# Kernel tuning notes

Hardware: AMD Instinct MI355X
Metric: run time of the kernel (lower is better)

## Reference

```python
import jax, jax.numpy as jnp
import numpy as np

B, N, K = 4, 2048, 32
U, TU = 512, 128
RADII = (0.1, 0.3, 0.5)
FILTERS = [512, 256, 170]  # U // (i+1) for depth=3
BN_RS = 1.0 / np.sqrt(1.0 + 1e-3)  # inference BN with mean=0, var=1, keras eps=1e-3


def setup_inputs() -> dict:
    key = jax.random.key(0)
    ks = jax.random.split(key, 16)
    rn = lambda k, shape, s: jax.random.normal(k, shape, jnp.float32) * s
    d = {
        "pts": jax.random.normal(ks[0], (B, N, 3), jnp.float32),
        # T-Net params
        "t_cw": rn(ks[1], (3, TU), 0.3), "t_cb": jnp.zeros((TU,), jnp.float32),
        "t_g1": jnp.ones((TU,), jnp.float32), "t_b1": jnp.zeros((TU,), jnp.float32),
        "t_d1w": rn(ks[2], (TU, TU), 0.1), "t_d1b": jnp.zeros((TU,), jnp.float32),
        "t_g2": jnp.ones((TU,), jnp.float32), "t_b2": jnp.zeros((TU,), jnp.float32),
        "t_d2w": rn(ks[3], (TU, 9), 0.3), "t_d2b": jnp.zeros((9,), jnp.float32),
        # PCE conv1 + residual conv
        "c1_w": rn(ks[4], (9, U), 0.2), "c1_b": jnp.zeros((U,), jnp.float32),
        "c1_g": jnp.ones((U,), jnp.float32), "c1_beta": jnp.zeros((U,), jnp.float32),
        "res_w": rn(ks[5], (U, U), 0.05), "res_b": jnp.zeros((U,), jnp.float32),
    }
    fin = U
    for i, f in enumerate(FILTERS):
        d[f"blk{i}_w"] = rn(ks[6 + i], (fin, f), 0.05)
        d[f"blk{i}_b"] = jnp.zeros((f,), jnp.float32)
        d[f"blk{i}_g"] = jnp.ones((f,), jnp.float32)
        d[f"blk{i}_beta"] = jnp.zeros((f,), jnp.float32)
        fin = f
    return d


def _bn(x, g, b):
    # inference BN with moving_mean=0, moving_var=1: (x-0)/sqrt(1+eps)*g + b
    return x * (BN_RS * g) + b


def reference(pts, t_cw, t_cb, t_g1, t_b1, t_d1w, t_d1b, t_g2, t_b2, t_d2w, t_d2b,
              c1_w, c1_b, c1_g, c1_beta, res_w, res_b,
              blk0_w, blk0_b, blk0_g, blk0_beta,
              blk1_w, blk1_b, blk1_g, blk1_beta,
              blk2_w, blk2_b, blk2_g, blk2_beta):
    silu = jax.nn.silu  # keras 'swish'
    # ---- OrthogonalTNet (dropout = identity at inference) ----
    x = silu(_bn(jnp.einsum('bnd,de->bne', pts, t_cw) + t_cb, t_g1, t_b1))  # [B,N,TU]
    x = x.max(axis=1)                                                        # GlobalMaxPool1D
    x = silu(_bn(x @ t_d1w + t_d1b, t_g2, t_b2))
    T = (x @ t_d2w + t_d2b).reshape(-1, 3, 3)
    pc = jnp.einsum('bnd,bde->bne', pts, T)                                  # [B,N,3]
    # ---- pairwise distances [B,N,N] ----
    sq = jnp.sum(pc * pc, axis=-1)
    d2 = sq[:, :, None] + sq[:, None, :] - 2.0 * jnp.einsum('bnd,bmd->bnm', pc, pc)
    dist = jnp.sqrt(jnp.maximum(d2, 0.0))
    # ---- multi-scale grouping: radius mask -> top_k -> gather ----
    groups = []
    for r in RADII:
        mask = (dist <= r).astype(jnp.float32)
        idx = jax.lax.top_k(mask, K)[1]                                      # [B,N,K]
        groups.append(jax.vmap(lambda p, i: p[i])(pc, idx))                  # [B,N,K,3]
    f = jnp.concatenate(groups, axis=-1)                                     # [B,N,K,9]
    # ---- 1x1 conv stack (Dense over channel dim), dropout = identity ----
    f = silu(_bn(f @ c1_w + c1_b, c1_g, c1_beta))                            # [B,N,K,U]
    f = f + (f @ res_w + res_b)                                              # residual
    for w, b, g, beta in ((blk0_w, blk0_b, blk0_g, blk0_beta),
                          (blk1_w, blk1_b, blk1_g, blk1_beta),
                          (blk2_w, blk2_b, blk2_g, blk2_beta)):
        f = silu(_bn(f @ w + b, g, beta))
    Bv, Nv, Kv, Cv = f.shape
    f = f.reshape(Bv, Nv, Kv * Cv)                                           # [B,N,K*170]
    return f.max(axis=1)                                                     # GlobalMaxPool1D -> [B,5440]
```

## Files before the change

kernel.cpp:

```cpp
#include <hip/hip_runtime.h>
#include <math.h>

#define BN_RS 0.9995003746877732f

typedef unsigned short u16;
typedef _Float16 f16;
typedef __attribute__((ext_vector_type(8))) _Float16 h8v;
typedef __attribute__((ext_vector_type(4))) _Float16 h4v;
typedef __attribute__((ext_vector_type(2))) __fp16 fp16x2;
typedef __attribute__((ext_vector_type(4))) float f32x4;
typedef __attribute__((ext_vector_type(16))) float f32x16;

__device__ __forceinline__ unsigned f2mono(float f){
  unsigned u = __float_as_uint(f);
  return (u & 0x80000000u) ? ~u : (u | 0x80000000u);
}
__device__ __forceinline__ float mono2f(unsigned m){
  unsigned u = (m & 0x80000000u) ? (m & 0x7FFFFFFFu) : ~m;
  return __uint_as_float(u);
}
__device__ __forceinline__ float silu_fast(float x){
  float e = __expf(-x);
  return x * __builtin_amdgcn_rcpf(1.f + e);
}
__device__ __forceinline__ float silu_f64(float x){
  double e = exp(-(double)x);
  return (float)((double)x / (1.0 + e));
}
__device__ __forceinline__ h4v pkrtz4(float a, float b, float c, float d){
  fp16x2 lo = __builtin_amdgcn_cvt_pkrtz(a, b);
  fp16x2 hi = __builtin_amdgcn_cvt_pkrtz(c, d);
  unsigned lu = __builtin_bit_cast(unsigned, lo);
  unsigned hu = __builtin_bit_cast(unsigned, hi);
  unsigned long long packed = ((unsigned long long)hu << 32) | lu;
  return __builtin_bit_cast(h4v, packed);
}

constexpr size_t OFF_T9   = 0;
constexpr size_t OFF_XM   = 1024;
constexpr size_t OFF_PC4  = 4096;
constexpr size_t OFF_OUT  = 139264;
constexpr size_t OFF_C1T  = 227328;
constexpr size_t OFF_B0C  = 262144;
constexpr size_t OFF_B1T  = 1310720;
constexpr size_t OFF_B2T  = 1572864;
constexpr size_t OFF_BS1  = 1662976;
constexpr size_t OFF_BS0  = 1667072;
constexpr size_t OFF_BSB1 = 1669120;
constexpr size_t OFF_BSB2 = 1670144;
constexpr size_t OFF_F9   = 1703936;

__global__ void tnet1_kernel(const float* __restrict__ pts, const float* __restrict__ t_cw,
                             const float* __restrict__ t_cb, const float* __restrict__ t_g1,
                             const float* __restrict__ t_b1, unsigned* __restrict__ xm_mono){
  int u = threadIdx.x;
  int b = blockIdx.x;
  int slice = blockIdx.y * blockDim.y + threadIdx.y;
  float w0 = t_cw[u], w1 = t_cw[128+u], w2 = t_cw[256+u];
  float cb = t_cb[u];
  float sc = __fmul_rn(BN_RS, t_g1[u]);
  float b1 = t_b1[u];
  float mx = -INFINITY;
  const float* P = pts + ((size_t)b*2048 + (size_t)slice*128)*3;
  for (int n = 0; n < 128; ++n){
    float y = __fadd_rn(__fadd_rn(__fmul_rn(P[n*3+0], w0), __fmul_rn(P[n*3+1], w1)),
                        __fmul_rn(P[n*3+2], w2));
    y = __fadd_rn(y, cb);
    y = __fadd_rn(__fmul_rn(y, sc), b1);
    mx = fmaxf(mx, silu_f64(y));
  }
  atomicMax(&xm_mono[b*128+u], f2mono(mx));
}

__global__ void tnet2_kernel(const unsigned* __restrict__ xm_mono,
                             const float* __restrict__ d1w, const float* __restrict__ d1b,
                             const float* __restrict__ g2, const float* __restrict__ b2,
                             const float* __restrict__ d2w, const float* __restrict__ d2b,
                             float* __restrict__ T9){
  __shared__ float xs[128], x2s[128];
  int u = threadIdx.x, b = blockIdx.x;
  xs[u] = mono2f(xm_mono[b*128+u]);
  __syncthreads();
  double acc = (double)d1b[u];
  for (int v = 0; v < 128; ++v) acc += (double)xs[v] * (double)d1w[v*128+u];
  double sc = (double)__fmul_rn(BN_RS, g2[u]);
  acc = acc*sc + (double)b2[u];
  double e = exp(-acc);
  x2s[u] = (float)(acc / (1.0 + e));
  __syncthreads();
  if (u < 9){
    double t = (double)d2b[u];
    for (int v = 0; v < 128; ++v) t += (double)x2s[v] * (double)d2w[v*9+u];
    T9[b*9+u] = (float)t;
  }
}

__global__ void pc_kernel(const float* __restrict__ pts, const float* __restrict__ T9,
                          float4* __restrict__ pc4){
  int i = blockIdx.x*blockDim.x + threadIdx.x;
  int b = i >> 11;
  const float* p = pts + (size_t)i*3;
  float x = p[0], y = p[1], z = p[2];
  const float* T = T9 + b*9;
  float px = __fadd_rn(__fadd_rn(__fmul_rn(x, T[0]), __fmul_rn(y, T[3])), __fmul_rn(z, T[6]));
  float py = __fadd_rn(__fadd_rn(__fmul_rn(x, T[1]), __fmul_rn(y, T[4])), __fmul_rn(z, T[7]));
  float pz = __fadd_rn(__fadd_rn(__fmul_rn(x, T[2]), __fmul_rn(y, T[5])), __fmul_rn(z, T[8]));
  float sq = __fadd_rn(__fadd_rn(__fmul_rn(px, px), __fmul_rn(py, py)), __fmul_rn(pz, pz));
  pc4[i] = make_float4(px, py, pz, sq);
}

__global__ __launch_bounds__(256) void group_kernel(const float4* __restrict__ pc4,
                                                    f16* __restrict__ f9){
  __shared__ int ones[4][3][32];
  __shared__ int zer [4][3][32];
  const float RAD[3] = {0.1f, 0.3f, 0.5f};
  int tid = threadIdx.x, wave = tid >> 6, lane = tid & 63;
  int bid = blockIdx.x;
  int b = bid >> 9, n0 = (bid & 511) * 4;
  const float4* src = pc4 + (size_t)b*2048;

  int n = n0 + wave;
  float4 pi = src[n];
  float xi = pi.x, yi = pi.y, zi = pi.z, sqi = pi.w;
  int c1[3] = {0,0,0}, c0[3] = {0,0,0};
  unsigned long long lt = (1ULL << lane) - 1ULL;

  for (int ch = 0; ch < 32; ++ch){
    int j = ch*64 + lane;
    float4 pj = src[j];
    float dot = __fadd_rn(__fadd_rn(__fmul_rn(xi, pj.x), __fmul_rn(yi, pj.y)),
                          __fmul_rn(zi, pj.z));
    float d2 = __fsub_rn(__fadd_rn(sqi, pj.w), __fmul_rn(2.f, dot));
    float dist = sqrtf(fmaxf(d2, 0.f));
    #pragma unroll
    for (int ri = 0; ri < 3; ++ri){
      bool in = (dist <= RAD[ri]);
      unsigned long long m = __ballot(in);
      int pc_lt = (int)__popcll(m & lt);
      if (c1[ri] < 32){
        int pos = c1[ri] + pc_lt;
        if (in && pos < 32) ones[wave][ri][pos] = j;
      }
      if (c0[ri] < 32){
        int pos = c0[ri] + (int)(lane - pc_lt);
        if (!in && pos < 32) zer[wave][ri][pos] = j;
      }
      int t1 = (int)__popcll(m);
      c1[ri] += t1;
      c0[ri] += 64 - t1;
    }
    if (c1[0] >= 32 && c1[1] >= 32 && c1[2] >= 32 &&
        c0[0] >= 32 && c0[1] >= 32 && c0[2] >= 32) break;
  }

  if (lane < 32){
    h8v va, vb;
    #pragma unroll
    for (int t = 0; t < 8; ++t){ va[t] = (f16)0.f; vb[t] = (f16)0.f; }
    #pragma unroll
    for (int ri = 0; ri < 3; ++ri){
      int cc = c1[ri] < 32 ? c1[ri] : 32;
      int sel = (lane < cc) ? ones[wave][ri][lane] : zer[wave][ri][lane - cc];
      float4 p = src[sel];
      if (ri == 0){ va[0]=(f16)p.x; va[1]=(f16)p.y; va[2]=(f16)p.z; }
      if (ri == 1){ va[3]=(f16)p.x; va[4]=(f16)p.y; va[5]=(f16)p.z; }
      if (ri == 2){ va[6]=(f16)p.x; va[7]=(f16)p.y; vb[0]=(f16)p.z; }
    }
    f16* dst = f9 + (((size_t)(b*2048 + n) * 32 + lane) << 4);
    *(h8v*)dst = va;
    *(h8v*)(dst + 8) = vb;
  }
}

__device__ __forceinline__ void pack_frag32(const float* __restrict__ src, f16* __restrict__ dst,
                                            int CO, int CI, int COr, int CIr,
                                            const float* __restrict__ g,
                                            int i0, int stride){
  int NT16 = CI >> 4;
  int total = (CO >> 5) * NT16 * 512;
  for (int x = i0; x < total; x += stride){
    int j = x & 7, lane = (x >> 3) & 63;
    int t = (x >> 9) % NT16, sct = x / (NT16 << 9);
    int co = sct*32 + (lane & 31);
    int ci = t*16 + ((lane >> 5) << 3) + j;
    float v = 0.f;
    if (co < COr && ci < CIr){
      v = src[ci*COr + co];
      if (g) v *= BN_RS * g[co];
    }
    dst[x] = (f16)v;
  }
}
__device__ __forceinline__ void pack_frag16(const float* __restrict__ src, f16* __restrict__ dst,
                                            int CO, int CI, int COr, int CIr,
                                            const float* __restrict__ g,
                                            int i0, int stride){
  int NT = CI >> 5;
  int total = (CO >> 4) * NT * 512;
  for (int x = i0; x < total; x += stride){
    int j = x & 7, lane = (x >> 3) & 63;
    int t = (x >> 9) % NT, sct = x / (NT << 9);
    int co = sct*16 + (lane & 15);
    int ci = t*32 + (lane >> 4)*8 + j;
    float v = 0.f;
    if (co < COr && ci < CIr){
      v = src[ci*COr + co];
      if (g) v *= BN_RS * g[co];
    }
    dst[x] = (f16)v;
  }
}

__global__ void prep_kernel(const float* __restrict__ c1w,
                            const float* __restrict__ b0w, const float* __restrict__ b1w,
                            const float* __restrict__ b2w,
                            const float* __restrict__ c1_b, const float* __restrict__ c1_g, const float* __restrict__ c1_be,
                            const float* __restrict__ res_b,
                            const float* __restrict__ b0_b, const float* __restrict__ b0_g, const float* __restrict__ b0_be,
                            const float* __restrict__ b1_b, const float* __restrict__ b1_g, const float* __restrict__ b1_be,
                            const float* __restrict__ b2_b, const float* __restrict__ b2_g, const float* __restrict__ b2_be,
                            f16* __restrict__ c1F, f16* __restrict__ b1F, f16* __restrict__ b2F,
                            float* __restrict__ bs1, float* __restrict__ bs0,
                            float* __restrict__ bsb1, float* __restrict__ bsb2){
  int i0 = blockIdx.x*blockDim.x + threadIdx.x;
  int stride = gridDim.x*blockDim.x;
  pack_frag32(c1w,  c1F,  512,  32, 512,   9, c1_g, i0, stride);
  pack_frag32(b1w,  b1F,  256, 512, 256, 512, b1_g, i0, stride);
  pack_frag16(b2w,  b2F,  176, 256, 170, 256, b2_g, i0, stride);
  for (int x = i0; x < 512; x += stride){
    bs1[x] = c1_b[x]*(BN_RS*c1_g[x]) + c1_be[x];
    float s = b0_b[x];
    for (int m = 0; m < 512; ++m) s = fmaf(res_b[m], b0w[m*512 + x], s);
    bs0[x] = s*(BN_RS*b0_g[x]) + b0_be[x];
  }
  for (int x = i0; x < 256; x += stride) bsb1[x] = b1_b[x]*(BN_RS*b1_g[x]) + b1_be[x];
  for (int x = i0; x < 176; x += stride)
    bsb2[x] = (x < 170) ? b2_b[x]*(BN_RS*b2_g[x]) + b2_be[x] : 0.f;
}

__global__ __launch_bounds__(256) void composeb0_kernel(const float* __restrict__ resw,
                                                        const float* __restrict__ b0w,
                                                        const float* __restrict__ b0_g,
                                                        f16* __restrict__ b0C){
  __shared__ float Rt[64][129];
  __shared__ float Wt[128][17];
  const int tid = threadIdx.x;
  const int co0 = (blockIdx.x & 31) * 16;
  const int ci0 = (blockIdx.x >> 5) * 64;
  const int r  = tid >> 2;
  const int cq = tid & 3;
  float acc[4] = {0.f, 0.f, 0.f, 0.f};

  for (int mc = 0; mc < 512; mc += 128){
    {
      int row = tid >> 2, mb = (tid & 3) * 32;
      const float* src = resw + (size_t)(ci0 + row)*512 + mc + mb;
      #pragma unroll
      for (int i = 0; i < 8; ++i){
        float4 v = *(const float4*)(src + i*4);
        Rt[row][mb + i*4 + 0] = v.x; Rt[row][mb + i*4 + 1] = v.y;
        Rt[row][mb + i*4 + 2] = v.z; Rt[row][mb + i*4 + 3] = v.w;
      }
    }
    {
      int m = tid >> 1, c8 = (tid & 1) * 8;
      const float* src = b0w + (size_t)(mc + m)*512 + co0 + c8;
      float4 v0 = *(const float4*)(src);
      float4 v1 = *(const float4*)(src + 4);
      Wt[m][c8+0] = v0.x; Wt[m][c8+1] = v0.y; Wt[m][c8+2] = v0.z; Wt[m][c8+3] = v0.w;
      Wt[m][c8+4] = v1.x; Wt[m][c8+5] = v1.y; Wt[m][c8+6] = v1.z; Wt[m][c8+7] = v1.w;
    }
    __syncthreads();
    #pragma unroll 8
    for (int m = 0; m < 128; ++m){
      float rv = Rt[r][m];
      #pragma unroll
      for (int i = 0; i < 4; ++i)
        acc[i] = fmaf(rv, Wt[m][cq*4 + i], acc[i]);
    }
    __syncthreads();
  }
  int ci = ci0 + r;
  #pragma unroll
  for (int i = 0; i < 4; ++i){
    int co = co0 + cq*4 + i;
    float s = acc[i] + b0w[(size_t)ci*512 + co];
    s *= BN_RS * b0_g[co];
    int sct = co >> 5, t = ci >> 4;
    int lane = (co & 31) | (((ci >> 3) & 1) << 5);
    int j = ci & 7;
    b0C[((size_t)(sct*32 + t)*64 + lane)*8 + j] = (f16)s;
  }
}

__device__ __forceinline__ int swzb(int row, int c){
  return (row*1024 + c*2) ^ ((row & 7) << 4);
}

template<int NT16, int NCT>
__device__ __forceinline__ void mm32(const char* actc, const f16* __restrict__ WF,
                                     int sct0, int lane, f32x16 (&acc)[NCT]){
  const int ln = lane & 31, hi = lane >> 5;
  const int xr = (ln & 7) << 4;
  #pragma unroll
  for (int t = 0; t < NT16; ++t){
    int koff = (t*32 + (hi << 4)) ^ xr;
    h8v a = *(const h8v*)(actc + ln*1024 + koff);
    #pragma unroll
    for (int ct = 0; ct < NCT; ++ct){
      h8v w = *(const h8v*)&WF[((size_t)((sct0 + ct)*NT16 + t)*64 + lane)*8];
      acc[ct] = __builtin_amdgcn_mfma_f32_32x32x16_f16(w, a, acc[ct], 0, 0, 0);
    }
  }
}

template<int NCT>
__device__ __forceinline__ void epi32(char* outc, int co0, const float* __restrict__ bias,
                                      int lane, f32x16 (&acc)[NCT]){
  const int ln = lane & 31, hi = lane >> 5;
  #pragma unroll
  for (int ct = 0; ct < NCT; ++ct){
    #pragma unroll
    for (int q = 0; q < 4; ++q){
      int ch = co0 + ct*32 + q*8 + hi*4;
      float4 b4 = *(const float4*)(bias + ch);
      *(h4v*)(outc + swzb(ln, ch)) = pkrtz4(
          silu_fast(acc[ct][q*4+0] + b4.x),
          silu_fast(acc[ct][q*4+1] + b4.y),
          silu_fast(acc[ct][q*4+2] + b4.z),
          silu_fast(acc[ct][q*4+3] + b4.w));
    }
  }
}

__global__ __launch_bounds__(512, 4) void mlp_kernel(
    const f16* __restrict__ f9,
    const f16* __restrict__ c1F, const f16* __restrict__ b0C,
    const f16* __restrict__ b1F, const f16* __restrict__ b2F,
    const float* __restrict__ bs1, const float* __restrict__ bs0,
    const float* __restrict__ bsb1, const float* __restrict__ bsb2,
    unsigned* __restrict__ outmax){
  __shared__ __align__(16) f16 bufA[32*512];
  __shared__ __align__(16) f16 bufB[32*512];
  char* A = (char*)bufA;
  char* B = (char*)bufB;
  const int tid  = threadIdx.x;
  const int wave = tid >> 6, lane = tid & 63;
  const int ln = lane & 31, hi = lane >> 5;
  const int lrow = lane & 15, lkg = lane >> 4;
  const int bid = blockIdx.x;
  const int b = bid >> 11, k = (bid >> 6) & 31, n0 = (bid & 63) << 5;

  if (tid < 128){
    int row = tid >> 2, part = tid & 3;
    h8v v;
    if (part < 2){
      const f16* src = f9 + (((size_t)(b*2048 + n0 + row) * 32 + k) << 4) + part*8;
      v = *(const h8v*)src;
    } else {
      #pragma unroll
      for (int t = 0; t < 8; ++t) v[t] = (f16)0.f;
    }
    *(h8v*)&bufA[row*32 + part*8] = v;
  }
  __syncthreads();

  const f32x16 zf16 = {0.f,0.f,0.f,0.f,0.f,0.f,0.f,0.f,0.f,0.f,0.f,0.f,0.f,0.f,0.f,0.f};
  f32x16 acc[2];

  acc[0] = zf16; acc[1] = zf16;
  #pragma unroll
  for (int t = 0; t < 2; ++t){
    h8v a = *(const h8v*)(A + ln*64 + t*32 + hi*16);
    #pragma unroll
    for (int ct = 0; ct < 2; ++ct){
      h8v w = *(const h8v*)&c1F[((size_t)((wave*2 + ct)*2 + t)*64 + lane)*8];
      acc[ct] = __builtin_amdgcn_mfma_f32_32x32x16_f16(w, a, acc[ct], 0, 0, 0);
    }
  }
  epi32<2>(B, wave*64, bs1, lane, acc);
  __syncthreads();

  acc[0] = zf16; acc[1] = zf16;
  mm32<32, 2>(B, b0C, wave*2, lane, acc);
  epi32<2>(A, wave*64, bs0, lane, acc);
  __syncthreads();

  f32x16 acc1[1];
  acc1[0] = zf16;
  mm32<32, 1>(A, b1F, wave, lane, acc1);
  epi32<1>(B, wave*32, bsb1, lane, acc1);
  __syncthreads();

  const f32x4 zf = {0.f, 0.f, 0.f, 0.f};
  f32x4 acc3[2][2];
  #pragma unroll
  for (int mt = 0; mt < 2; ++mt){ acc3[mt][0] = zf; acc3[mt][1] = zf; }
  {
    const int xr = (lrow & 7) << 4;
    const bool has2 = wave < 3;
    #pragma unroll
    for (int t = 0; t < 8; ++t){
      h8v a[2];
      int koff = ((t*4 + lkg) << 4) ^ xr;
      #pragma unroll
      for (int mt = 0; mt < 2; ++mt)
        a[mt] = *(const h8v*)(B + (mt*16 + lrow)*1024 + koff);
      {
        h8v w = *(const h8v*)&b2F[((size_t)(wave*8 + t)*64 + lane)*8];
        #pragma unroll
        for (int mt = 0; mt < 2; ++mt)
          acc3[mt][0] = __builtin_amdgcn_mfma_f32_16x16x32_f16(a[mt], w, acc3[mt][0], 0, 0, 0);
      }
      if (has2){
        h8v w = *(const h8v*)&b2F[((size_t)((wave + 8)*8 + t)*64 + lane)*8];
        #pragma unroll
        for (int mt = 0; mt < 2; ++mt)
          acc3[mt][1] = __builtin_amdgcn_mfma_f32_16x16x32_f16(a[mt], w, acc3[mt][1], 0, 0, 0);
      }
    }
    #pragma unroll
    for (int t = 0; t < 2; ++t){
      if (t == 1 && !has2) break;
      int c = ((t == 0) ? wave : wave + 8)*16 + lrow;
      if (c < 170){
        float bb = bsb2[c];
        float mx = -INFINITY;
        #pragma unroll
        for (int mt = 0; mt < 2; ++mt)
          #pragma unroll
          for (int rg = 0; rg < 4; ++rg)
            mx = fmaxf(mx, silu_fast(acc3[mt][t][rg] + bb));
        mx = fmaxf(mx, __shfl_xor(mx, 16));
        mx = fmaxf(mx, __shfl_xor(mx, 32));
        if (lkg == 0)
          atomicMax(&outmax[b*5440 + k*170 + c], f2mono(mx));
      }
    }
  }
}

__global__ void finalize_kernel(const unsigned* __restrict__ m, float* __restrict__ out, int n){
  int i = blockIdx.x*blockDim.x + threadIdx.x;
  if (i < n) out[i] = mono2f(m[i]);
}

extern "C" void kernel_launch(void* const* d_in, const int* in_sizes, int n_in,
                              void* d_out, int out_size, void* d_ws, size_t ws_size,
                              hipStream_t stream){
  const float* pts    = (const float*)d_in[0];
  const float* t_cw   = (const float*)d_in[1];
  const float* t_cb   = (const float*)d_in[2];
  const float* t_g1   = (const float*)d_in[3];
  const float* t_b1   = (const float*)d_in[4];
  const float* t_d1w  = (const float*)d_in[5];
  const float* t_d1b  = (const float*)d_in[6];
  const float* t_g2   = (const float*)d_in[7];
  const float* t_b2   = (const float*)d_in[8];
  const float* t_d2w  = (const float*)d_in[9];
  const float* t_d2b  = (const float*)d_in[10];
  const float* c1_w   = (const float*)d_in[11];
  const float* c1_b   = (const float*)d_in[12];
  const float* c1_g   = (const float*)d_in[13];
  const float* c1_be  = (const float*)d_in[14];
  const float* res_w  = (const float*)d_in[15];
  const float* res_b  = (const float*)d_in[16];
  const float* b0_w   = (const float*)d_in[17];
  const float* b0_b   = (const float*)d_in[18];
  const float* b0_g   = (const float*)d_in[19];
  const float* b0_be  = (const float*)d_in[20];
  const float* b1_w   = (const float*)d_in[21];
  const float* b1_b   = (const float*)d_in[22];
  const float* b1_g   = (const float*)d_in[23];
  const float* b1_be  = (const float*)d_in[24];
  const float* b2_w   = (const float*)d_in[25];
  const float* b2_b   = (const float*)d_in[26];
  const float* b2_g   = (const float*)d_in[27];
  const float* b2_be  = (const float*)d_in[28];

  char* ws = (char*)d_ws;
  float*    T9   = (float*)(ws + OFF_T9);
  unsigned* XM   = (unsigned*)(ws + OFF_XM);
  float4*   PC4  = (float4*)(ws + OFF_PC4);
  unsigned* OUTM = (unsigned*)(ws + OFF_OUT);
  f16* C1F  = (f16*)(ws + OFF_C1T);
  f16* B0C  = (f16*)(ws + OFF_B0C);
  f16* B1F  = (f16*)(ws + OFF_B1T);
  f16* B2F  = (f16*)(ws + OFF_B2T);
  float* BS1  = (float*)(ws + OFF_BS1);
  float* BS0  = (float*)(ws + OFF_BS0);
  float* BSB1 = (float*)(ws + OFF_BSB1);
  float* BSB2 = (float*)(ws + OFF_BSB2);
  f16* F9   = (f16*)(ws + OFF_F9);

  hipMemsetAsync(ws + OFF_XM, 0, 4*128*4, stream);
  hipMemsetAsync(ws + OFF_OUT, 0, 21760*4, stream);

  prep_kernel<<<512, 256, 0, stream>>>(c1_w, b0_w, b1_w, b2_w,
                                       c1_b, c1_g, c1_be, res_b,
                                       b0_b, b0_g, b0_be,
                                       b1_b, b1_g, b1_be,
                                       b2_b, b2_g, b2_be,
                                       C1F, B1F, B2F,
                                       BS1, BS0, BSB1, BSB2);
  composeb0_kernel<<<256, 256, 0, stream>>>(res_w, b0_w, b0_g, B0C);
  tnet1_kernel<<<dim3(4,4), dim3(128,4), 0, stream>>>(pts, t_cw, t_cb, t_g1, t_b1, XM);
  tnet2_kernel<<<4, 128, 0, stream>>>(XM, t_d1w, t_d1b, t_g2, t_b2, t_d2w, t_d2b, T9);
  pc_kernel<<<32, 256, 0, stream>>>(pts, T9, PC4);
  group_kernel<<<2048, 256, 0, stream>>>(PC4, F9);
  mlp_kernel<<<8192, 512, 0, stream>>>(F9, C1F, B0C, B1F, B2F,
                                       BS1, BS0, BSB1, BSB2, OUTM);
  finalize_kernel<<<(out_size + 255)/256, 256, 0, stream>>>(OUTM, (float*)d_out, out_size);
}
```

Baseline: 466.4 us.

## Process 64 points per MLP block to reuse each weight fragment twice

Doubles the row tile of the fused MLP kernel from 32 to 64 points, so each weight fragment loaded from global memory feeds two MFMAs instead of one. The grid is halved, the shared buffers double to 64 KB each, and launch bounds drop to 2 blocks per CU. This targets weight-load bandwidth and latency in the GEMM chain, at the cost of more registers, more LDS per block and lower occupancy.

```diff
diff --git a/kernel.cpp b/kernel.cpp
--- a/kernel.cpp
+++ b/kernel.cpp
@@ -298,25 +298,27 @@
 }
 
 template<int NT16, int NCT>
-__device__ __forceinline__ void mm32(const char* actc, const f16* __restrict__ WF,
-                                     int sct0, int lane, f32x16 (&acc)[NCT]){
+__device__ __forceinline__ void mm32x2(const char* actc, const f16* __restrict__ WF,
+                                       int sct0, int lane, f32x16 (&acc)[2][NCT]){
   const int ln = lane & 31, hi = lane >> 5;
   const int xr = (ln & 7) << 4;
   #pragma unroll
   for (int t = 0; t < NT16; ++t){
     int koff = (t*32 + (hi << 4)) ^ xr;
-    h8v a = *(const h8v*)(actc + ln*1024 + koff);
+    h8v a0 = *(const h8v*)(actc + ln*1024 + koff);
+    h8v a1 = *(const h8v*)(actc + (32 + ln)*1024 + koff);
     #pragma unroll
     for (int ct = 0; ct < NCT; ++ct){
       h8v w = *(const h8v*)&WF[((size_t)((sct0 + ct)*NT16 + t)*64 + lane)*8];
-      acc[ct] = __builtin_amdgcn_mfma_f32_32x32x16_f16(w, a, acc[ct], 0, 0, 0);
+      acc[0][ct] = __builtin_amdgcn_mfma_f32_32x32x16_f16(w, a0, acc[0][ct], 0, 0, 0);
+      acc[1][ct] = __builtin_amdgcn_mfma_f32_32x32x16_f16(w, a1, acc[1][ct], 0, 0, 0);
     }
   }
 }
 
 template<int NCT>
-__device__ __forceinline__ void epi32(char* outc, int co0, const float* __restrict__ bias,
-                                      int lane, f32x16 (&acc)[NCT]){
+__device__ __forceinline__ void epi32x2(char* outc, int co0, const float* __restrict__ bias,
+                                        int lane, f32x16 (&acc)[2][NCT]){
   const int ln = lane & 31, hi = lane >> 5;
   #pragma unroll
   for (int ct = 0; ct < NCT; ++ct){
@@ -324,24 +326,28 @@
     for (int q = 0; q < 4; ++q){
       int ch = co0 + ct*32 + q*8 + hi*4;
       float4 b4 = *(const float4*)(bias + ch);
-      *(h4v*)(outc + swzb(ln, ch)) = pkrtz4(
-          silu_fast(acc[ct][q*4+0] + b4.x),
-          silu_fast(acc[ct][q*4+1] + b4.y),
-          silu_fast(acc[ct][q*4+2] + b4.z),
-          silu_fast(acc[ct][q*4+3] + b4.w));
-    }
-  }
-}
-
-__global__ __launch_bounds__(512, 4) void mlp_kernel(
+      #pragma unroll
+      for (int mt = 0; mt < 2; ++mt){
+        int row = mt*32 + ln;
+        *(h4v*)(outc + swzb(row, ch)) = pkrtz4(
+            silu_fast(acc[mt][ct][q*4+0] + b4.x),
+            silu_fast(acc[mt][ct][q*4+1] + b4.y),
+            silu_fast(acc[mt][ct][q*4+2] + b4.z),
+            silu_fast(acc[mt][ct][q*4+3] + b4.w));
+      }
+    }
+  }
+}
+
+__global__ __launch_bounds__(512, 2) void mlp_kernel(
     const f16* __restrict__ f9,
     const f16* __restrict__ c1F, const f16* __restrict__ b0C,
     const f16* __restrict__ b1F, const f16* __restrict__ b2F,
     const float* __restrict__ bs1, const float* __restrict__ bs0,
     const float* __restrict__ bsb1, const float* __restrict__ bsb2,
     unsigned* __restrict__ outmax){
-  __shared__ __align__(16) f16 bufA[32*512];
-  __shared__ __align__(16) f16 bufB[32*512];
+  __shared__ __align__(16) f16 bufA[64*512];
+  __shared__ __align__(16) f16 bufB[64*512];
   char* A = (char*)bufA;
   char* B = (char*)bufB;
   const int tid  = threadIdx.x;
@@ -349,9 +355,9 @@
   const int ln = lane & 31, hi = lane >> 5;
   const int lrow = lane & 15, lkg = lane >> 4;
   const int bid = blockIdx.x;
-  const int b = bid >> 11, k = (bid >> 6) & 31, n0 = (bid & 63) << 5;
-
-  if (tid < 128){
+  const int b = bid >> 10, k = (bid >> 5) & 31, n0 = (bid & 31) << 6;
+
+  if (tid < 256){
     int row = tid >> 2, part = tid & 3;
     h8v v;
     if (part < 2){
@@ -366,56 +372,58 @@
   __syncthreads();
 
   const f32x16 zf16 = {0.f,0.f,0.f,0.f,0.f,0.f,0.f,0.f,0.f,0.f,0.f,0.f,0.f,0.f,0.f,0.f};
-  f32x16 acc[2];
-
-  acc[0] = zf16; acc[1] = zf16;
+  f32x16 acc[2][2];
+
+  acc[0][0] = zf16; acc[0][1] = zf16; acc[1][0] = zf16; acc[1][1] = zf16;
   #pragma unroll
   for (int t = 0; t < 2; ++t){
-    h8v a = *(const h8v*)(A + ln*64 + t*32 + hi*16);
+    h8v a0 = *(const h8v*)(A + ln*64 + t*32 + hi*16);
+    h8v a1 = *(const h8v*)(A + (32 + ln)*64 + t*32 + hi*16);
     #pragma unroll
     for (int ct = 0; ct < 2; ++ct){
       h8v w = *(const h8v*)&c1F[((size_t)((wave*2 + ct)*2 + t)*64 + lane)*8];
-      acc[ct] = __builtin_amdgcn_mfma_f32_32x32x16_f16(w, a, acc[ct], 0, 0, 0);
-    }
-  }
-  epi32<2>(B, wave*64, bs1, lane, acc);
+      acc[0][ct] = __builtin_amdgcn_mfma_f32_32x32x16_f16(w, a0, acc[0][ct], 0, 0, 0);
+      acc[1][ct] = __builtin_amdgcn_mfma_f32_32x32x16_f16(w, a1, acc[1][ct], 0, 0, 0);
+    }
+  }
+  epi32x2<2>(B, wave*64, bs1, lane, acc);
   __syncthreads();
 
-  acc[0] = zf16; acc[1] = zf16;
-  mm32<32, 2>(B, b0C, wave*2, lane, acc);
-  epi32<2>(A, wave*64, bs0, lane, acc);
+  acc[0][0] = zf16; acc[0][1] = zf16; acc[1][0] = zf16; acc[1][1] = zf16;
+  mm32x2<32, 2>(B, b0C, wave*2, lane, acc);
+  epi32x2<2>(A, wave*64, bs0, lane, acc);
   __syncthreads();
 
-  f32x16 acc1[1];
-  acc1[0] = zf16;
-  mm32<32, 1>(A, b1F, wave, lane, acc1);
-  epi32<1>(B, wave*32, bsb1, lane, acc1);
+  f32x16 acc1[2][1];
+  acc1[0][0] = zf16; acc1[1][0] = zf16;
+  mm32x2<32, 1>(A, b1F, wave, lane, acc1);
+  epi32x2<1>(B, wave*32, bsb1, lane, acc1);
   __syncthreads();
 
   const f32x4 zf = {0.f, 0.f, 0.f, 0.f};
-  f32x4 acc3[2][2];
+  f32x4 acc3[4][2];
   #pragma unroll
-  for (int mt = 0; mt < 2; ++mt){ acc3[mt][0] = zf; acc3[mt][1] = zf; }
+  for (int mt = 0; mt < 4; ++mt){ acc3[mt][0] = zf; acc3[mt][1] = zf; }
   {
     const int xr = (lrow & 7) << 4;
     const bool has2 = wave < 3;
     #pragma unroll
     for (int t = 0; t < 8; ++t){
-      h8v a[2];
+      h8v a[4];
       int koff = ((t*4 + lkg) << 4) ^ xr;
       #pragma unroll
-      for (int mt = 0; mt < 2; ++mt)
+      for (int mt = 0; mt < 4; ++mt)
         a[mt] = *(const h8v*)(B + (mt*16 + lrow)*1024 + koff);
       {
         h8v w = *(const h8v*)&b2F[((size_t)(wave*8 + t)*64 + lane)*8];
         #pragma unroll
-        for (int mt = 0; mt < 2; ++mt)
+        for (int mt = 0; mt < 4; ++mt)
           acc3[mt][0] = __builtin_amdgcn_mfma_f32_16x16x32_f16(a[mt], w, acc3[mt][0], 0, 0, 0);
       }
       if (has2){
         h8v w = *(const h8v*)&b2F[((size_t)((wave + 8)*8 + t)*64 + lane)*8];
         #pragma unroll
-        for (int mt = 0; mt < 2; ++mt)
+        for (int mt = 0; mt < 4; ++mt)
           acc3[mt][1] = __builtin_amdgcn_mfma_f32_16x16x32_f16(a[mt], w, acc3[mt][1], 0, 0, 0);
       }
     }
@@ -427,7 +435,7 @@
         float bb = bsb2[c];
         float mx = -INFINITY;
         #pragma unroll
-        for (int mt = 0; mt < 2; ++mt)
+        for (int mt = 0; mt < 4; ++mt)
           #pragma unroll
           for (int rg = 0; rg < 4; ++rg)
             mx = fmaxf(mx, silu_fast(acc3[mt][t][rg] + bb));
@@ -508,7 +516,7 @@
   tnet2_kernel<<<4, 128, 0, stream>>>(XM, t_d1w, t_d1b, t_g2, t_b2, t_d2w, t_d2b, T9);
   pc_kernel<<<32, 256, 0, stream>>>(pts, T9, PC4);
   group_kernel<<<2048, 256, 0, stream>>>(PC4, F9);
-  mlp_kernel<<<8192, 512, 0, stream>>>(F9, C1F, B0C, B1F, B2F,
+  mlp_kernel<<<4096, 512, 0, stream>>>(F9, C1F, B0C, B1F, B2F,
                                        BS1, BS0, BSB1, BSB2, OUTM);
   finalize_kernel<<<(out_size + 255)/256, 256, 0, stream>>>(OUTM, (float*)d_out, out_size);
 }
```

Measured after the change: 454.1 us. -2.6%, faster.
